# Kernel tuning notes

Hardware: AMD Instinct MI355X
Metric: run time of the kernel (lower is better)

The kernel has to match this reference:

```python
import jax, jax.numpy as jnp
import numpy as np

NUM_USERS = 100000
NUM_ITEMS = 50000
EMB_DIM = 128
N_EDGES = 1600000
BATCH = 16384
L_USER = (0, 1, 2)


def setup_inputs() -> dict:
    key = jax.random.key(0)
    k1, k2, k3, k4, k5, k6 = jax.random.split(key, 6)
    users = jax.random.randint(k1, (BATCH,), 0, NUM_USERS)
    items = jax.random.randint(k2, (BATCH,), 0, NUM_ITEMS)
    edge_src = jax.random.randint(k3, (N_EDGES,), 0, NUM_USERS)
    edge_dst = jax.random.randint(k4, (N_EDGES,), 0, NUM_USERS)
    # nn.Parameter init: normal(mean=0, std=0.01)
    user_emb = jax.random.normal(k5, (NUM_USERS, EMB_DIM), dtype=jnp.float32) * 0.01
    item_emb = jax.random.normal(k6, (NUM_ITEMS, EMB_DIM), dtype=jnp.float32) * 0.01
    return {"users": users, "items": items, "edge_src": edge_src,
            "edge_dst": edge_dst, "user_emb": user_emb, "item_emb": item_emb}


def social_conv(edge_src, edge_dst, h):
    # DGL copy_u -> mean aggregation over social (user-user) edges
    msgs = h[edge_src]  # [E, D] gather
    agg = jax.ops.segment_sum(msgs, edge_dst, num_segments=NUM_USERS)  # [N, D]
    deg = jax.ops.segment_sum(jnp.ones_like(edge_dst, dtype=h.dtype), edge_dst,
                              num_segments=NUM_USERS)  # [N]
    return agg / jnp.maximum(deg, 1.0)[:, None]


def reference(users, items, edge_src, edge_dst, user_emb, item_emb):
    g1 = social_conv(edge_src, edge_dst, user_emb)
    g2 = social_conv(edge_src, edge_dst, g1)
    final_user = jnp.zeros_like(user_emb)
    if 0 in L_USER:
        final_user = final_user + user_emb
    if 1 in L_USER:
        final_user = final_user + g1
    if 2 in L_USER:
        final_user = final_user + g2
    latest_user = final_user[users]   # [B, D]
    latest_item = item_emb[items]     # [B, D]
    predict = jax.nn.sigmoid(jnp.sum(latest_user * latest_item, axis=1))  # [B]
    return predict, latest_user, latest_item
```

## Files before the change

kernel.cpp:

```cpp
#include <hip/hip_runtime.h>
#include <math.h>

#define NUM_USERS 100000
#define NUM_ITEMS 50000
#define EMB_D 128
#define N_EDGES 1600000
#define BATCH 16384

#define NBINS 391
#define BIN_CAP 8192
#define CHUNK 4096
#define NCHUNKS 391

#define CVT_BLOCKS 12500

#define FP8_SCALE 512.0f
#define FP8_INV   (1.0f / 512.0f)

typedef unsigned short u16;
typedef unsigned int   u32;
typedef float f32x2 __attribute__((ext_vector_type(2)));

__device__ __forceinline__ f32x2 fp8pair_dec(u16 p) {
    return __builtin_amdgcn_cvt_pk_f32_fp8((int)p, false);
}

__global__ void prep_kernel(const float* __restrict__ in, u32* __restrict__ outp,
                            int* __restrict__ bin_cursor) {
    int blk = blockIdx.x;
    if (blk < CVT_BLOCKS) {
        long long i = (long long)blk * 256 + threadIdx.x;
        float4 a = *(const float4*)(in + i * 4);
        int r = __builtin_amdgcn_cvt_pk_fp8_f32(a.x * FP8_SCALE, a.y * FP8_SCALE, 0, false);
        r = __builtin_amdgcn_cvt_pk_fp8_f32(a.z * FP8_SCALE, a.w * FP8_SCALE, r, true);
        outp[i] = (u32)r;
    } else {
        for (int i = threadIdx.x; i < 512; i += 256) bin_cursor[i] = i * BIN_CAP;
    }
}

__global__ void partition_kernel(const int* __restrict__ edge_src, const int* __restrict__ edge_dst,
                                 int* __restrict__ bin_cursor, u32* __restrict__ coarse) {
    __shared__ int hist[NBINS];
    __shared__ int cnt2[NBINS];
    __shared__ int base[NBINS];
    __shared__ int sdst[CHUNK];
    int tid = threadIdx.x;
    long long c0 = (long long)blockIdx.x * CHUNK;
    int n = (int)min((long long)CHUNK, (long long)N_EDGES - c0);
    for (int i = tid; i < NBINS; i += 256) { hist[i] = 0; cnt2[i] = 0; }
    __syncthreads();
    for (int i = tid; i < n; i += 256) {
        int d = edge_dst[c0 + i];
        sdst[i] = d;
        atomicAdd(&hist[d >> 8], 1);
    }
    __syncthreads();
    for (int i = tid; i < NBINS; i += 256) {
        int h = hist[i];
        if (h) base[i] = atomicAdd(&bin_cursor[i], h);
    }
    __syncthreads();
    for (int i = tid; i < n; i += 256) {
        int d = sdst[i];
        int b = d >> 8;
        int idx = atomicAdd(&cnt2[b], 1);
        int pos = base[b] + idx;
        if (pos >= b * BIN_CAP && pos < (b + 1) * BIN_CAP)
            coarse[pos] = ((u32)edge_src[c0 + i] << 8) | (u32)(d & 255);
    }
}

__global__ void fine_kernel(const int* __restrict__ bin_cursor, const u32* __restrict__ coarse,
                            int* __restrict__ sorted_src, int* __restrict__ counts,
                            int* __restrict__ row_start) {
    __shared__ int scnt[256];
    __shared__ int soff[256];
    int b = blockIdx.x;
    int tid = threadIdx.x;
    int binBase = b << 8;
    int s = b * BIN_CAP;
    int e = min(bin_cursor[b], (b + 1) * BIN_CAP);
    scnt[tid] = 0;
    __syncthreads();
    for (int i = s + tid; i < e; i += 256) atomicAdd(&scnt[coarse[i] & 255u], 1);
    __syncthreads();
    int v = scnt[tid];
    soff[tid] = v;
    __syncthreads();
    #pragma unroll
    for (int off = 1; off < 256; off <<= 1) {
        int t = (tid >= off) ? soff[tid - off] : 0;
        __syncthreads();
        soff[tid] += t;
        __syncthreads();
    }
    int rs = s + soff[tid] - v;
    int user = binBase + tid;
    if (user < NUM_USERS) {
        counts[user] = v;
        row_start[user] = rs;
    }
    scnt[tid] = rs;
    __syncthreads();
    for (int i = s + tid; i < e; i += 256) {
        u32 p = coarse[i];
        int pos = atomicAdd(&scnt[p & 255u], 1);
        sorted_src[pos] = (int)(p >> 8);
    }
}

__global__ void agg_kernel(const int* __restrict__ row_start, const int* __restrict__ counts,
                           const int* __restrict__ sorted_src, const u16* __restrict__ tab,
                           u16* __restrict__ outp) {
    int wid = (blockIdx.x * blockDim.x + threadIdx.x) >> 6;
    int lane = threadIdx.x & 63;
    if (wid >= NUM_USERS) return;
    wid = __builtin_amdgcn_readfirstlane(wid);
    int cnt = counts[wid];
    int start = row_start[wid];
    float ax = 0.f, ay = 0.f;
    int j = 0;
    for (; j + 8 <= cnt; j += 8) {
        int ss[8];
        #pragma unroll
        for (int k = 0; k < 8; k++) ss[k] = sorted_src[start + j + k];
        u16 pp[8];
        #pragma unroll
        for (int k = 0; k < 8; k++) pp[k] = tab[(long long)ss[k] * 64 + lane];
        #pragma unroll
        for (int k = 0; k < 8; k++) {
            f32x2 d = fp8pair_dec(pp[k]);
            ax += d.x; ay += d.y;
        }
    }
    if (j < cnt) {
        int ss[8];
        #pragma unroll
        for (int k = 0; k < 8; k++) {
            int idx = min(j + k, cnt - 1);
            ss[k] = sorted_src[start + idx];
        }
        u16 pp[8];
        #pragma unroll
        for (int k = 0; k < 8; k++) pp[k] = tab[(long long)ss[k] * 64 + lane];
        #pragma unroll
        for (int k = 0; k < 8; k++) {
            f32x2 d = fp8pair_dec(pp[k]);
            float w = (j + k < cnt) ? 1.0f : 0.0f;
            ax += d.x * w; ay += d.y * w;
        }
    }
    float inv = 1.0f / fmaxf((float)cnt, 1.0f);
    int enc = __builtin_amdgcn_cvt_pk_fp8_f32(ax * inv, ay * inv, 0, false);
    outp[(long long)wid * 64 + lane] = (u16)enc;
}

__global__ void final_kernel(const int* __restrict__ users, const int* __restrict__ items,
                             const float* __restrict__ user_emb, const float* __restrict__ item_emb,
                             const u16* __restrict__ g18, const int* __restrict__ row_start,
                             const int* __restrict__ counts, const int* __restrict__ sorted_src,
                             float* __restrict__ out_predict, float* __restrict__ out_lu,
                             float* __restrict__ out_li) {
    int b = (blockIdx.x * blockDim.x + threadIdx.x) >> 6;
    int lane = threadIdx.x & 63;
    if (b >= BATCH) return;
    b = __builtin_amdgcn_readfirstlane(b);
    int u = users[b];
    int it = items[b];
    int cnt = counts[u];
    int start = row_start[u];
    float ax = 0.f, ay = 0.f;
    int j = 0;
    for (; j + 8 <= cnt; j += 8) {
        int ss[8];
        #pragma unroll
        for (int k = 0; k < 8; k++) ss[k] = sorted_src[start + j + k];
        u16 pp[8];
        #pragma unroll
        for (int k = 0; k < 8; k++) pp[k] = g18[(long long)ss[k] * 64 + lane];
        #pragma unroll
        for (int k = 0; k < 8; k++) {
            f32x2 d = fp8pair_dec(pp[k]);
            ax += d.x; ay += d.y;
        }
    }
    if (j < cnt) {
        int ss[8];
        #pragma unroll
        for (int k = 0; k < 8; k++) {
            int idx = min(j + k, cnt - 1);
            ss[k] = sorted_src[start + idx];
        }
        u16 pp[8];
        #pragma unroll
        for (int k = 0; k < 8; k++) pp[k] = g18[(long long)ss[k] * 64 + lane];
        #pragma unroll
        for (int k = 0; k < 8; k++) {
            f32x2 d = fp8pair_dec(pp[k]);
            float w = (j + k < cnt) ? 1.0f : 0.0f;
            ax += d.x * w; ay += d.y * w;
        }
    }
    float inv = (1.0f / fmaxf((float)cnt, 1.0f)) * FP8_INV;
    float2 ue = *(const float2*)(user_emb + (long long)u * EMB_D + lane * 2);
    f32x2 a1 = fp8pair_dec(g18[(long long)u * 64 + lane]);
    float2 ie = *(const float2*)(item_emb + (long long)it * EMB_D + lane * 2);
    float2 lu;
    lu.x = ue.x + a1.x * FP8_INV + ax * inv;
    lu.y = ue.y + a1.y * FP8_INV + ay * inv;
    *(float2*)(out_lu + (long long)b * EMB_D + lane * 2) = lu;
    *(float2*)(out_li + (long long)b * EMB_D + lane * 2) = ie;
    float dot = lu.x * ie.x + lu.y * ie.y;
    #pragma unroll
    for (int off = 32; off > 0; off >>= 1) dot += __shfl_down(dot, off, 64);
    if (lane == 0) out_predict[b] = 1.0f / (1.0f + expf(-dot));
}

extern "C" void kernel_launch(void* const* d_in, const int* in_sizes, int n_in,
                              void* d_out, int out_size, void* d_ws, size_t ws_size,
                              hipStream_t stream) {
    const int* users     = (const int*)d_in[0];
    const int* items     = (const int*)d_in[1];
    const int* edge_src  = (const int*)d_in[2];
    const int* edge_dst  = (const int*)d_in[3];
    const float* user_emb = (const float*)d_in[4];
    const float* item_emb = (const float*)d_in[5];

    const int PADDED = NBINS * BIN_CAP;

    int* ws_i = (int*)d_ws;
    int* bin_cursor = ws_i;
    int* counts     = bin_cursor + 512;
    int* row_start  = counts + 100352;
    int* sorted_src = row_start + 100352;
    u32* coarse     = (u32*)(sorted_src + PADDED);
    u32* ue8 = coarse + PADDED;
    u32* g18 = ue8 + 3200000;

    float* out_predict = (float*)d_out;
    float* out_lu = out_predict + BATCH;
    float* out_li = out_lu + (long long)BATCH * EMB_D;

    prep_kernel<<<CVT_BLOCKS + 1, 256, 0, stream>>>(user_emb, ue8, bin_cursor);

    partition_kernel<<<NCHUNKS, 256, 0, stream>>>(edge_src, edge_dst, bin_cursor, coarse);
    fine_kernel<<<NBINS, 256, 0, stream>>>(bin_cursor, coarse, sorted_src, counts, row_start);

    agg_kernel<<<(NUM_USERS + 3) / 4, 256, 0, stream>>>(
        row_start, counts, sorted_src, (const u16*)ue8, (u16*)g18);

    final_kernel<<<(BATCH + 3) / 4, 256, 0, stream>>>(
        users, items, user_emb, item_emb, (const u16*)g18, row_start, counts, sorted_src,
        out_predict, out_lu, out_li);
}
```

Baseline: 224.0 us.

## Fuse fp8 conversion with edge partition and gather 4-byte rows using half-wave edge pairs

The fp8 table conversion and the coarse edge partition now run in one launch, with the bin counters zeroed by a memset. This lets the independent conversion blocks overlap with the partition blocks. The gather kernels now load 4 fp8 values per lane as u32 over 32 lanes, with each half-wave handling a different neighbour, and combine the halves with a cross-half shuffle. This halves the number of wide gather instructions per edge and doubles edges in flight, at the cost of extra shuffles and one more tiny memset launch.

```diff
diff --git a/kernel.cpp b/kernel.cpp
--- a/kernel.cpp
+++ b/kernel.cpp
@@ -21,32 +21,24 @@
 typedef unsigned int   u32;
 typedef float f32x2 __attribute__((ext_vector_type(2)));
 
-__device__ __forceinline__ f32x2 fp8pair_dec(u16 p) {
-    return __builtin_amdgcn_cvt_pk_f32_fp8((int)p, false);
-}
-
-__global__ void prep_kernel(const float* __restrict__ in, u32* __restrict__ outp,
-                            int* __restrict__ bin_cursor) {
+__global__ void prep_part_kernel(const float* __restrict__ in, u32* __restrict__ outp,
+                                 const int* __restrict__ edge_src, const int* __restrict__ edge_dst,
+                                 int* __restrict__ bin_cnt, u32* __restrict__ coarse) {
+    __shared__ int hist[NBINS];
+    __shared__ int cnt2[NBINS];
+    __shared__ int base[NBINS];
+    __shared__ int sdst[CHUNK];
     int blk = blockIdx.x;
-    if (blk < CVT_BLOCKS) {
-        long long i = (long long)blk * 256 + threadIdx.x;
+    if (blk >= NCHUNKS) {
+        long long i = (long long)(blk - NCHUNKS) * 256 + threadIdx.x;
         float4 a = *(const float4*)(in + i * 4);
         int r = __builtin_amdgcn_cvt_pk_fp8_f32(a.x * FP8_SCALE, a.y * FP8_SCALE, 0, false);
         r = __builtin_amdgcn_cvt_pk_fp8_f32(a.z * FP8_SCALE, a.w * FP8_SCALE, r, true);
         outp[i] = (u32)r;
-    } else {
-        for (int i = threadIdx.x; i < 512; i += 256) bin_cursor[i] = i * BIN_CAP;
-    }
-}
-
-__global__ void partition_kernel(const int* __restrict__ edge_src, const int* __restrict__ edge_dst,
-                                 int* __restrict__ bin_cursor, u32* __restrict__ coarse) {
-    __shared__ int hist[NBINS];
-    __shared__ int cnt2[NBINS];
-    __shared__ int base[NBINS];
-    __shared__ int sdst[CHUNK];
+        return;
+    }
     int tid = threadIdx.x;
-    long long c0 = (long long)blockIdx.x * CHUNK;
+    long long c0 = (long long)blk * CHUNK;
     int n = (int)min((long long)CHUNK, (long long)N_EDGES - c0);
     for (int i = tid; i < NBINS; i += 256) { hist[i] = 0; cnt2[i] = 0; }
     __syncthreads();
@@ -58,20 +50,20 @@
     __syncthreads();
     for (int i = tid; i < NBINS; i += 256) {
         int h = hist[i];
-        if (h) base[i] = atomicAdd(&bin_cursor[i], h);
+        if (h) base[i] = atomicAdd(&bin_cnt[i], h);
     }
     __syncthreads();
     for (int i = tid; i < n; i += 256) {
         int d = sdst[i];
         int b = d >> 8;
         int idx = atomicAdd(&cnt2[b], 1);
-        int pos = base[b] + idx;
-        if (pos >= b * BIN_CAP && pos < (b + 1) * BIN_CAP)
-            coarse[pos] = ((u32)edge_src[c0 + i] << 8) | (u32)(d & 255);
-    }
-}
-
-__global__ void fine_kernel(const int* __restrict__ bin_cursor, const u32* __restrict__ coarse,
+        int pl = base[b] + idx;
+        if (pl >= 0 && pl < BIN_CAP)
+            coarse[(long long)b * BIN_CAP + pl] = ((u32)edge_src[c0 + i] << 8) | (u32)(d & 255);
+    }
+}
+
+__global__ void fine_kernel(const int* __restrict__ bin_cnt, const u32* __restrict__ coarse,
                             int* __restrict__ sorted_src, int* __restrict__ counts,
                             int* __restrict__ row_start) {
     __shared__ int scnt[256];
@@ -80,7 +72,7 @@
     int tid = threadIdx.x;
     int binBase = b << 8;
     int s = b * BIN_CAP;
-    int e = min(bin_cursor[b], (b + 1) * BIN_CAP);
+    int e = s + min(bin_cnt[b], BIN_CAP);
     scnt[tid] = 0;
     __syncthreads();
     for (int i = s + tid; i < e; i += 256) atomicAdd(&scnt[coarse[i] & 255u], 1);
@@ -111,54 +103,71 @@
 }
 
 __global__ void agg_kernel(const int* __restrict__ row_start, const int* __restrict__ counts,
-                           const int* __restrict__ sorted_src, const u16* __restrict__ tab,
-                           u16* __restrict__ outp) {
+                           const int* __restrict__ sorted_src, const u32* __restrict__ tab32,
+                           u32* __restrict__ out32) {
     int wid = (blockIdx.x * blockDim.x + threadIdx.x) >> 6;
     int lane = threadIdx.x & 63;
     if (wid >= NUM_USERS) return;
     wid = __builtin_amdgcn_readfirstlane(wid);
     int cnt = counts[wid];
     int start = row_start[wid];
-    float ax = 0.f, ay = 0.f;
+    int dlane = lane & 31;
+    int hi = lane >> 5;
+    float4 acc = make_float4(0.f, 0.f, 0.f, 0.f);
     int j = 0;
-    for (; j + 8 <= cnt; j += 8) {
-        int ss[8];
-        #pragma unroll
-        for (int k = 0; k < 8; k++) ss[k] = sorted_src[start + j + k];
-        u16 pp[8];
-        #pragma unroll
-        for (int k = 0; k < 8; k++) pp[k] = tab[(long long)ss[k] * 64 + lane];
-        #pragma unroll
-        for (int k = 0; k < 8; k++) {
-            f32x2 d = fp8pair_dec(pp[k]);
-            ax += d.x; ay += d.y;
+    for (; j + 16 <= cnt; j += 16) {
+        int rr[8];
+        #pragma unroll
+        for (int k = 0; k < 8; k++) {
+            int s0 = sorted_src[start + j + 2 * k];
+            int s1 = sorted_src[start + j + 2 * k + 1];
+            rr[k] = hi ? s1 : s0;
+        }
+        u32 pp[8];
+        #pragma unroll
+        for (int k = 0; k < 8; k++) pp[k] = tab32[(long long)rr[k] * 32 + dlane];
+        #pragma unroll
+        for (int k = 0; k < 8; k++) {
+            f32x2 d0 = __builtin_amdgcn_cvt_pk_f32_fp8((int)pp[k], false);
+            f32x2 d1 = __builtin_amdgcn_cvt_pk_f32_fp8((int)pp[k], true);
+            acc.x += d0.x; acc.y += d0.y; acc.z += d1.x; acc.w += d1.y;
         }
     }
     if (j < cnt) {
-        int ss[8];
-        #pragma unroll
-        for (int k = 0; k < 8; k++) {
-            int idx = min(j + k, cnt - 1);
-            ss[k] = sorted_src[start + idx];
-        }
-        u16 pp[8];
-        #pragma unroll
-        for (int k = 0; k < 8; k++) pp[k] = tab[(long long)ss[k] * 64 + lane];
-        #pragma unroll
-        for (int k = 0; k < 8; k++) {
-            f32x2 d = fp8pair_dec(pp[k]);
-            float w = (j + k < cnt) ? 1.0f : 0.0f;
-            ax += d.x * w; ay += d.y * w;
-        }
-    }
+        int rr[8]; float ww[8];
+        #pragma unroll
+        for (int k = 0; k < 8; k++) {
+            int i0 = min(j + 2 * k, cnt - 1);
+            int i1 = min(j + 2 * k + 1, cnt - 1);
+            int s0 = sorted_src[start + i0];
+            int s1 = sorted_src[start + i1];
+            rr[k] = hi ? s1 : s0;
+            ww[k] = ((j + 2 * k + hi) < cnt) ? 1.0f : 0.0f;
+        }
+        u32 pp[8];
+        #pragma unroll
+        for (int k = 0; k < 8; k++) pp[k] = tab32[(long long)rr[k] * 32 + dlane];
+        #pragma unroll
+        for (int k = 0; k < 8; k++) {
+            f32x2 d0 = __builtin_amdgcn_cvt_pk_f32_fp8((int)pp[k], false);
+            f32x2 d1 = __builtin_amdgcn_cvt_pk_f32_fp8((int)pp[k], true);
+            acc.x += d0.x * ww[k]; acc.y += d0.y * ww[k];
+            acc.z += d1.x * ww[k]; acc.w += d1.y * ww[k];
+        }
+    }
+    acc.x += __shfl_xor(acc.x, 32, 64);
+    acc.y += __shfl_xor(acc.y, 32, 64);
+    acc.z += __shfl_xor(acc.z, 32, 64);
+    acc.w += __shfl_xor(acc.w, 32, 64);
     float inv = 1.0f / fmaxf((float)cnt, 1.0f);
-    int enc = __builtin_amdgcn_cvt_pk_fp8_f32(ax * inv, ay * inv, 0, false);
-    outp[(long long)wid * 64 + lane] = (u16)enc;
+    int enc = __builtin_amdgcn_cvt_pk_fp8_f32(acc.x * inv, acc.y * inv, 0, false);
+    enc = __builtin_amdgcn_cvt_pk_fp8_f32(acc.z * inv, acc.w * inv, enc, true);
+    if (lane < 32) out32[(long long)wid * 32 + dlane] = (u32)enc;
 }
 
 __global__ void final_kernel(const int* __restrict__ users, const int* __restrict__ items,
                              const float* __restrict__ user_emb, const float* __restrict__ item_emb,
-                             const u16* __restrict__ g18, const int* __restrict__ row_start,
+                             const u32* __restrict__ g18, const int* __restrict__ row_start,
                              const int* __restrict__ counts, const int* __restrict__ sorted_src,
                              float* __restrict__ out_predict, float* __restrict__ out_lu,
                              float* __restrict__ out_li) {
@@ -170,50 +179,72 @@
     int it = items[b];
     int cnt = counts[u];
     int start = row_start[u];
-    float ax = 0.f, ay = 0.f;
+    int dlane = lane & 31;
+    int hi = lane >> 5;
+    float4 acc = make_float4(0.f, 0.f, 0.f, 0.f);
     int j = 0;
-    for (; j + 8 <= cnt; j += 8) {
-        int ss[8];
-        #pragma unroll
-        for (int k = 0; k < 8; k++) ss[k] = sorted_src[start + j + k];
-        u16 pp[8];
-        #pragma unroll
-        for (int k = 0; k < 8; k++) pp[k] = g18[(long long)ss[k] * 64 + lane];
-        #pragma unroll
-        for (int k = 0; k < 8; k++) {
-            f32x2 d = fp8pair_dec(pp[k]);
-            ax += d.x; ay += d.y;
+    for (; j + 16 <= cnt; j += 16) {
+        int rr[8];
+        #pragma unroll
+        for (int k = 0; k < 8; k++) {
+            int s0 = sorted_src[start + j + 2 * k];
+            int s1 = sorted_src[start + j + 2 * k + 1];
+            rr[k] = hi ? s1 : s0;
+        }
+        u32 pp[8];
+        #pragma unroll
+        for (int k = 0; k < 8; k++) pp[k] = g18[(long long)rr[k] * 32 + dlane];
+        #pragma unroll
+        for (int k = 0; k < 8; k++) {
+            f32x2 d0 = __builtin_amdgcn_cvt_pk_f32_fp8((int)pp[k], false);
+            f32x2 d1 = __builtin_amdgcn_cvt_pk_f32_fp8((int)pp[k], true);
+            acc.x += d0.x; acc.y += d0.y; acc.z += d1.x; acc.w += d1.y;
         }
     }
     if (j < cnt) {
-        int ss[8];
-        #pragma unroll
-        for (int k = 0; k < 8; k++) {
-            int idx = min(j + k, cnt - 1);
-            ss[k] = sorted_src[start + idx];
-        }
-        u16 pp[8];
-        #pragma unroll
-        for (int k = 0; k < 8; k++) pp[k] = g18[(long long)ss[k] * 64 + lane];
-        #pragma unroll
-        for (int k = 0; k < 8; k++) {
-            f32x2 d = fp8pair_dec(pp[k]);
-            float w = (j + k < cnt) ? 1.0f : 0.0f;
-            ax += d.x * w; ay += d.y * w;
-        }
-    }
+        int rr[8]; float ww[8];
+        #pragma unroll
+        for (int k = 0; k < 8; k++) {
+            int i0 = min(j + 2 * k, cnt - 1);
+            int i1 = min(j + 2 * k + 1, cnt - 1);
+            int s0 = sorted_src[start + i0];
+            int s1 = sorted_src[start + i1];
+            rr[k] = hi ? s1 : s0;
+            ww[k] = ((j + 2 * k + hi) < cnt) ? 1.0f : 0.0f;
+        }
+        u32 pp[8];
+        #pragma unroll
+        for (int k = 0; k < 8; k++) pp[k] = g18[(long long)rr[k] * 32 + dlane];
+        #pragma unroll
+        for (int k = 0; k < 8; k++) {
+            f32x2 d0 = __builtin_amdgcn_cvt_pk_f32_fp8((int)pp[k], false);
+            f32x2 d1 = __builtin_amdgcn_cvt_pk_f32_fp8((int)pp[k], true);
+            acc.x += d0.x * ww[k]; acc.y += d0.y * ww[k];
+            acc.z += d1.x * ww[k]; acc.w += d1.y * ww[k];
+        }
+    }
+    acc.x += __shfl_xor(acc.x, 32, 64);
+    acc.y += __shfl_xor(acc.y, 32, 64);
+    acc.z += __shfl_xor(acc.z, 32, 64);
+    acc.w += __shfl_xor(acc.w, 32, 64);
     float inv = (1.0f / fmaxf((float)cnt, 1.0f)) * FP8_INV;
-    float2 ue = *(const float2*)(user_emb + (long long)u * EMB_D + lane * 2);
-    f32x2 a1 = fp8pair_dec(g18[(long long)u * 64 + lane]);
-    float2 ie = *(const float2*)(item_emb + (long long)it * EMB_D + lane * 2);
-    float2 lu;
-    lu.x = ue.x + a1.x * FP8_INV + ax * inv;
-    lu.y = ue.y + a1.y * FP8_INV + ay * inv;
-    *(float2*)(out_lu + (long long)b * EMB_D + lane * 2) = lu;
-    *(float2*)(out_li + (long long)b * EMB_D + lane * 2) = ie;
-    float dot = lu.x * ie.x + lu.y * ie.y;
+    float4 ue = *(const float4*)(user_emb + (long long)u * EMB_D + dlane * 4);
+    u32 a1p = g18[(long long)u * 32 + dlane];
+    f32x2 a0 = __builtin_amdgcn_cvt_pk_f32_fp8((int)a1p, false);
+    f32x2 a1 = __builtin_amdgcn_cvt_pk_f32_fp8((int)a1p, true);
+    float4 ie = *(const float4*)(item_emb + (long long)it * EMB_D + dlane * 4);
+    float4 lu;
+    lu.x = ue.x + a0.x * FP8_INV + acc.x * inv;
+    lu.y = ue.y + a0.y * FP8_INV + acc.y * inv;
+    lu.z = ue.z + a1.x * FP8_INV + acc.z * inv;
+    lu.w = ue.w + a1.y * FP8_INV + acc.w * inv;
+    if (lane < 32) {
+        *(float4*)(out_lu + (long long)b * EMB_D + dlane * 4) = lu;
+        *(float4*)(out_li + (long long)b * EMB_D + dlane * 4) = ie;
+    }
+    float dot = lu.x * ie.x + lu.y * ie.y + lu.z * ie.z + lu.w * ie.w;
     #pragma unroll
-    for (int off = 32; off > 0; off >>= 1) dot += __shfl_down(dot, off, 64);
+    for (int off = 16; off > 0; off >>= 1) dot += __shfl_down(dot, off, 64);
     if (lane == 0) out_predict[b] = 1.0f / (1.0f + expf(-dot));
 }
 
@@ -230,8 +261,8 @@
     const int PADDED = NBINS * BIN_CAP;
 
     int* ws_i = (int*)d_ws;
-    int* bin_cursor = ws_i;
-    int* counts     = bin_cursor + 512;
+    int* bin_cnt    = ws_i;
+    int* counts     = bin_cnt + 512;
     int* row_start  = counts + 100352;
     int* sorted_src = row_start + 100352;
     u32* coarse     = (u32*)(sorted_src + PADDED);
@@ -242,15 +273,17 @@
     float* out_lu = out_predict + BATCH;
     float* out_li = out_lu + (long long)BATCH * EMB_D;
 
-    prep_kernel<<<CVT_BLOCKS + 1, 256, 0, stream>>>(user_emb, ue8, bin_cursor);
-
-    partition_kernel<<<NCHUNKS, 256, 0, stream>>>(edge_src, edge_dst, bin_cursor, coarse);
-    fine_kernel<<<NBINS, 256, 0, stream>>>(bin_cursor, coarse, sorted_src, counts, row_start);
+    hipMemsetAsync(bin_cnt, 0, 512 * sizeof(int), stream);
+
+    prep_part_kernel<<<NCHUNKS + CVT_BLOCKS, 256, 0, stream>>>(
+        user_emb, ue8, edge_src, edge_dst, bin_cnt, coarse);
+
+    fine_kernel<<<NBINS, 256, 0, stream>>>(bin_cnt, coarse, sorted_src, counts, row_start);
 
     agg_kernel<<<(NUM_USERS + 3) / 4, 256, 0, stream>>>(
-        row_start, counts, sorted_src, (const u16*)ue8, (u16*)g18);
+        row_start, counts, sorted_src, ue8, g18);
 
     final_kernel<<<(BATCH + 3) / 4, 256, 0, stream>>>(
-        users, items, user_emb, item_emb, (const u16*)g18, row_start, counts, sorted_src,
+        users, items, user_emb, item_emb, g18, row_start, counts, sorted_src,
         out_predict, out_lu, out_li);
 }
```

Measured after the change: 216.4 us. 1.03x faster.
